# Kernel tuning notes

Hardware: AMD Instinct MI355X
Metric: run time of the kernel (lower is better)

Reference implementation:

```python
import jax, jax.numpy as jnp
import numpy as np

FP8_MAX = 448.0  # max finite value of float8_e4m3fn


def _fp8_quant(v, scale):
    # emulate saturating scaled cast to float8_e4m3fn, then dequant-free fp8 storage (upcast to f32 for the gemm)
    q = jnp.clip(v / scale, -FP8_MAX, FP8_MAX)
    return q.astype(jnp.float8_e4m3fn).astype(jnp.float32)


def setup_inputs() -> dict:
    key = jax.random.key(0)
    k0, k1, k2, k3 = jax.random.split(key, 4)
    T, H, I, E = 1024, 1024, 2816, 8
    x = jax.random.normal(k0, (T, H), jnp.float32)
    router_logits = jax.random.normal(k1, (T, E), jnp.float32)
    w13_weight = jax.random.normal(k2, (E, 2 * I, H), jnp.float32) * 0.02
    w2_weight = jax.random.normal(k3, (E, H, I), jnp.float32) * 0.02
    return {
        "x": x,
        "router_logits": router_logits,
        "w13_weight": w13_weight,
        "w2_weight": w2_weight,
        "w13_input_scale": jnp.ones((E,), jnp.float32),
        "w2_input_scale": jnp.ones((E,), jnp.float32),
        "top_k": 2,
    }


def reference(x, router_logits, w13_weight, w2_weight, w13_input_scale, w2_input_scale, top_k):
    T, H = x.shape
    E, two_I, _ = w13_weight.shape
    I = two_I // 2

    # --- routing: softmax -> top_k -> renormalize (select_experts) ---
    probs = jax.nn.softmax(router_logits, axis=-1)
    topk_w, topk_ids = jax.lax.top_k(probs, top_k)            # [T,K]
    topk_w = topk_w / jnp.sum(topk_w, axis=-1, keepdims=True)
    # dense combine matrix [T,E]: sparsity of the grouped gemm dispatch
    combine = jnp.zeros((T, E), x.dtype).at[jnp.arange(T)[:, None], topk_ids].add(topk_w)

    # --- per-expert fp8 weight quantization (ops.scaled_fp8_quant per expert) ---
    w13_scale = jnp.max(jnp.abs(w13_weight), axis=(1, 2)) / FP8_MAX  # [E]
    w2_scale = jnp.max(jnp.abs(w2_weight), axis=(1, 2)) / FP8_MAX
    w13_q = _fp8_quant(w13_weight, w13_scale[:, None, None])         # [E,2I,H]
    w2_q = _fp8_quant(w2_weight, w2_scale[:, None, None])            # [E,H,I]

    # --- grouped gemm 1: per-expert activation quant + fp8 gemm + dequant scale ---
    x_q = _fp8_quant(x[None], w13_input_scale[:, None, None])        # [E,T,H]
    h = jnp.einsum('eth,eih->eti', x_q, w13_q) * (w13_input_scale * w13_scale)[:, None, None]

    # --- silu_and_mul: gate = first intermediate_size rows, up = second ---
    act = jax.nn.silu(h[..., :I]) * h[..., I:]                       # [E,T,I]

    # --- grouped gemm 2 ---
    act_q = _fp8_quant(act, w2_input_scale[:, None, None])
    o = jnp.einsum('eti,ehi->eth', act_q, w2_q) * (w2_input_scale * w2_scale)[:, None, None]

    # --- post_reorder: weighted combine of selected experts ---
    return jnp.einsum('te,eth->th', combine, o)                      # [T,H]
```

## Files before the change

kernel.cpp:

```cpp
#include <hip/hip_runtime.h>
#include <cstdint>
#include <cstddef>

#define T_TOK 1024
#define H_DIM 1024
#define I_DIM 2816
#define E_NUM 8
#define PAIRS 2048
#define KSPLIT 4
#define NT1 88
#define AMX2_X 32

typedef __attribute__((ext_vector_type(4))) float f32x4;
typedef __attribute__((ext_vector_type(4))) unsigned int u32x4;
typedef long i64;

__device__ __forceinline__ unsigned char fp8e4m3_sw(float v) {
  v = fminf(448.f, fmaxf(-448.f, v));
  unsigned b = __float_as_uint(v);
  unsigned s = (b >> 24) & 0x80u;
  float a = fabsf(v);
  if (a < 0.015625f) {
    int m = (int)rintf(a * 512.f);
    return (unsigned char)(s | (unsigned)m);
  }
  unsigned ab = b & 0x7fffffffu;
  unsigned rnd = 0x7FFFFu + ((ab >> 20) & 1u);
  ab += rnd;
  int e = (int)(ab >> 23) - 127;
  unsigned m = (ab >> 20) & 7u;
  if (e > 8 || (e == 8 && m > 6)) { e = 8; m = 6; }
  return (unsigned char)(s | (unsigned)((e + 7) << 3) | m);
}

__device__ __forceinline__ unsigned q4(float a, float b, float c, float d) {
#if __has_builtin(__builtin_amdgcn_cvt_pk_fp8_f32)
  unsigned w = (unsigned)__builtin_amdgcn_cvt_pk_fp8_f32(a, b, 0, false);
  return (unsigned)__builtin_amdgcn_cvt_pk_fp8_f32(c, d, (int)w, true);
#else
  return (unsigned)fp8e4m3_sw(a) | ((unsigned)fp8e4m3_sw(b) << 8) |
         ((unsigned)fp8e4m3_sw(c) << 16) | ((unsigned)fp8e4m3_sw(d) << 24);
#endif
}

__device__ __forceinline__ unsigned char q1(float a) {
#if __has_builtin(__builtin_amdgcn_cvt_pk_fp8_f32)
  return (unsigned char)((unsigned)__builtin_amdgcn_cvt_pk_fp8_f32(a, a, 0, false) & 0xFFu);
#else
  return fp8e4m3_sw(a);
#endif
}

__device__ __forceinline__ unsigned q4v(float4 f, float inv) {
  return q4(f.x * inv, f.y * inv, f.z * inv, f.w * inv);
}

__device__ __forceinline__ float wave_max(float m) {
#pragma unroll
  for (int off = 32; off > 0; off >>= 1) m = fmaxf(m, __shfl_xor(m, off));
  return m;
}

__global__ __launch_bounds__(256) void pre_k(const float* __restrict__ w13,
                                             const float* __restrict__ logits,
                                             float* __restrict__ part13,
                                             int* __restrict__ cnt_g,
                                             int* __restrict__ offs_g,
                                             int* __restrict__ pair_tok,
                                             float* __restrict__ pair_w,
                                             int* __restrict__ pairidx) {
  const int tid = threadIdx.x;
  if (blockIdx.x < 1024) {
    const int e = blockIdx.x >> 7, sub = blockIdx.x & 127;
    const float4* src = (const float4*)w13 + (size_t)e * (2 * I_DIM * H_DIM / 4);
    int idx = sub * 256 + tid;
    const int stride = 128 * 256;
    float m = 0.f;
#pragma unroll
    for (int j = 0; j < 44; j += 4) {
      float4 v0 = src[idx + (size_t)(j + 0) * stride];
      float4 v1 = src[idx + (size_t)(j + 1) * stride];
      float4 v2 = src[idx + (size_t)(j + 2) * stride];
      float4 v3 = src[idx + (size_t)(j + 3) * stride];
      m = fmaxf(m, fmaxf(fmaxf(fabsf(v0.x), fabsf(v0.y)), fmaxf(fabsf(v0.z), fabsf(v0.w))));
      m = fmaxf(m, fmaxf(fmaxf(fabsf(v1.x), fabsf(v1.y)), fmaxf(fabsf(v1.z), fabsf(v1.w))));
      m = fmaxf(m, fmaxf(fmaxf(fabsf(v2.x), fabsf(v2.y)), fmaxf(fabsf(v2.z), fabsf(v2.w))));
      m = fmaxf(m, fmaxf(fmaxf(fabsf(v3.x), fabsf(v3.y)), fmaxf(fabsf(v3.z), fabsf(v3.w))));
    }
    m = wave_max(m);
    __shared__ float wmax[4];
    int lane = tid & 63, wid = tid >> 6;
    if (lane == 0) wmax[wid] = m;
    __syncthreads();
    if (tid == 0)
      part13[blockIdx.x] = fmaxf(fmaxf(wmax[0], wmax[1]), fmaxf(wmax[2], wmax[3]));
    return;
  }

  __shared__ int cnt_s[E_NUM], pos_s[E_NUM];
  if (tid < E_NUM) cnt_s[tid] = 0;
  __syncthreads();
  int i0s[4], i1s[4];
  float w0s[4], w1s[4];
#pragma unroll
  for (int j = 0; j < 4; j++) {
    int t = tid * 4 + j;
    float l[E_NUM];
#pragma unroll
    for (int k = 0; k < E_NUM; k++) l[k] = logits[t * E_NUM + k];
    int i0 = 0; float b0 = l[0];
#pragma unroll
    for (int k = 1; k < E_NUM; k++) { if (l[k] > b0) { b0 = l[k]; i0 = k; } }
    int i1 = -1; float b1 = -3.4e38f;
#pragma unroll
    for (int k = 0; k < E_NUM; k++) { if (k != i0 && l[k] > b1) { b1 = l[k]; i1 = k; } }
    float e1 = expf(b1 - b0);
    float d = 1.f + e1;
    i0s[j] = i0; i1s[j] = i1; w0s[j] = 1.f / d; w1s[j] = e1 / d;
    atomicAdd(&cnt_s[i0], 1);
    atomicAdd(&cnt_s[i1], 1);
  }
  __syncthreads();
  if (tid == 0) {
    int s = 0;
#pragma unroll
    for (int e = 0; e < E_NUM; e++) {
      cnt_g[e] = cnt_s[e];
      offs_g[e] = s;
      pos_s[e] = s;
      s += cnt_s[e];
    }
    offs_g[E_NUM] = s;
  }
  __syncthreads();
#pragma unroll
  for (int j = 0; j < 4; j++) {
    int t = tid * 4 + j;
    int s0 = atomicAdd(&pos_s[i0s[j]], 1);
    pair_tok[s0] = t; pair_w[s0] = w0s[j]; pairidx[2 * t] = s0;
    int s1 = atomicAdd(&pos_s[i1s[j]], 1);
    pair_tok[s1] = t; pair_w[s1] = w1s[j]; pairidx[2 * t + 1] = s1;
  }
}

__global__ __launch_bounds__(256) void quantx_k(const float* __restrict__ x,
                                                const int* __restrict__ pair_tok,
                                                const int* __restrict__ offs,
                                                const float* __restrict__ s13,
                                                unsigned char* __restrict__ Xq) {
  int p = blockIdx.x;
  int t = pair_tok[p];
  int e = 0;
#pragma unroll
  for (int j = 1; j < E_NUM; j++) { if (p >= offs[j]) e = j; }
  float inv = 1.f / s13[e];
  float4 v = ((const float4*)(x + (size_t)t * H_DIM))[threadIdx.x];
  float a = fminf(448.f, fmaxf(-448.f, v.x * inv));
  float b = fminf(448.f, fmaxf(-448.f, v.y * inv));
  float c = fminf(448.f, fmaxf(-448.f, v.z * inv));
  float dd = fminf(448.f, fmaxf(-448.f, v.w * inv));
  ((unsigned*)(Xq + (size_t)p * H_DIM))[threadIdx.x] = q4(a, b, c, dd);
}

__global__ __launch_bounds__(256) void gemm1_k(const float* __restrict__ w13,
                                               const float* __restrict__ w2,
                                               const unsigned char* __restrict__ Xq,
                                               unsigned char* __restrict__ H1,
                                               const int* __restrict__ cnt,
                                               const int* __restrict__ offs,
                                               const float* __restrict__ part13,
                                               float* __restrict__ part2,
                                               const float* __restrict__ s13,
                                               const float* __restrict__ s2in) {
  const int e = blockIdx.z;
  const int tid = threadIdx.x, lane = tid & 63, wq = tid >> 6;

  if (blockIdx.x >= 2 * NT1) {
    const int bx2 = (blockIdx.x - 2 * NT1) * 4 + blockIdx.y;
    const float4* src = (const float4*)w2 + (size_t)e * (H_DIM * I_DIM / 4);
    int idx = bx2 * 256 + tid;
    const int stride = 128 * 256;
    float m = 0.f;
#pragma unroll
    for (int j = 0; j < 22; j++) {
      float4 v = src[idx + (size_t)j * stride];
      m = fmaxf(m, fmaxf(fmaxf(fabsf(v.x), fabsf(v.y)), fmaxf(fabsf(v.z), fabsf(v.w))));
    }
    m = wave_max(m);
    __shared__ float wmax2[4];
    if (lane == 0) wmax2[wq] = m;
    __syncthreads();
    if (tid == 0) {
      float mm = fmaxf(fmaxf(wmax2[0], wmax2[1]), fmaxf(wmax2[2], wmax2[3]));
      part2[e * 128 + bx2] = mm;
    }
    return;
  }

  __shared__ float redA[4];
  {
    float v = part13[e * 128 + (tid & 127)];
    v = wave_max(v);
    if (lane == 0) redA[wq] = v;
  }
  __syncthreads();
  float amax = fmaxf(fmaxf(redA[0], redA[1]), fmaxf(redA[2], redA[3]));

  const int bid = blockIdx.x;
  const int nt = (bid & 7) + (bid >> 4) * 8;
  const int mhalf = (bid >> 3) & 1;
  const int m0 = (blockIdx.y * 2 + mhalf) * 128;
  const int count = cnt[e];
  if (m0 >= count) return;
  const int base = offs[e];

  const float inv_w = 448.f / amax;
  const float gs = s13[e] * (amax / 448.f);
  const float inv_a2 = 1.f / s2in[e];

  __shared__ __align__(16) unsigned char As[128][80];
  __shared__ __align__(16) unsigned char Bs[64][80];

  const int fr = lane & 15, ks = lane >> 4;

  f32x4 accg[2][2], accu[2][2];
#pragma unroll
  for (int i = 0; i < 2; i++)
#pragma unroll
    for (int j = 0; j < 2; j++) { accg[i][j] = (f32x4)0.f; accu[i][j] = (f32x4)0.f; }

  const int ar0 = tid >> 2, aseg = tid & 3;
  int pr0 = base + m0 + ar0;      if (pr0 > PAIRS - 1) pr0 = PAIRS - 1;
  int pr1 = base + m0 + ar0 + 64; if (pr1 > PAIRS - 1) pr1 = PAIRS - 1;
  const unsigned char* a_src0 = Xq + (size_t)pr0 * H_DIM + aseg * 16;
  const unsigned char* a_src1 = Xq + (size_t)pr1 * H_DIM + aseg * 16;

  const int brow = tid >> 3, bseg = tid & 7;
  const float* bg_src = w13 + ((size_t)e * 2 * I_DIM + (size_t)nt * 32 + brow) * H_DIM + bseg * 8;
  const float* bu_src = bg_src + (size_t)I_DIM * H_DIM;

  u32x4 ra0 = *(const u32x4*)a_src0;
  u32x4 ra1 = *(const u32x4*)a_src1;
  float4 fg0 = ((const float4*)bg_src)[0], fg1 = ((const float4*)bg_src)[1];
  float4 fu0 = ((const float4*)bu_src)[0], fu1 = ((const float4*)bu_src)[1];
  unsigned qg0 = q4v(fg0, inv_w), qg1 = q4v(fg1, inv_w);
  unsigned qu0 = q4v(fu0, inv_w), qu1 = q4v(fu1, inv_w);

  for (int t = 0; t < H_DIM / 64; ++t) {
    __syncthreads();
    *(u32x4*)&As[ar0][aseg * 16] = ra0;
    *(u32x4*)&As[ar0 + 64][aseg * 16] = ra1;
    ((unsigned*)&Bs[brow][bseg * 8])[0] = qg0;
    ((unsigned*)&Bs[brow][bseg * 8])[1] = qg1;
    ((unsigned*)&Bs[32 + brow][bseg * 8])[0] = qu0;
    ((unsigned*)&Bs[32 + brow][bseg * 8])[1] = qu1;
    __syncthreads();
    if (t + 1 < H_DIM / 64) {
      int k0 = (t + 1) * 64;
      ra0 = *(const u32x4*)(a_src0 + k0);
      ra1 = *(const u32x4*)(a_src1 + k0);
      fg0 = ((const float4*)(bg_src + k0))[0];
      fg1 = ((const float4*)(bg_src + k0))[1];
      fu0 = ((const float4*)(bu_src + k0))[0];
      fu1 = ((const float4*)(bu_src + k0))[1];
    }
#pragma unroll
    for (int kk = 0; kk < 2; kk++) {
      i64 a0 = *(const i64*)&As[wq * 32 + fr][kk * 32 + ks * 8];
      i64 a1 = *(const i64*)&As[wq * 32 + 16 + fr][kk * 32 + ks * 8];
#pragma unroll
      for (int ni = 0; ni < 2; ni++) {
        i64 bg = *(const i64*)&Bs[ni * 16 + fr][kk * 32 + ks * 8];
        i64 bu = *(const i64*)&Bs[32 + ni * 16 + fr][kk * 32 + ks * 8];
        accg[0][ni] = __builtin_amdgcn_mfma_f32_16x16x32_fp8_fp8(a0, bg, accg[0][ni], 0, 0, 0);
        accg[1][ni] = __builtin_amdgcn_mfma_f32_16x16x32_fp8_fp8(a1, bg, accg[1][ni], 0, 0, 0);
        accu[0][ni] = __builtin_amdgcn_mfma_f32_16x16x32_fp8_fp8(a0, bu, accu[0][ni], 0, 0, 0);
        accu[1][ni] = __builtin_amdgcn_mfma_f32_16x16x32_fp8_fp8(a1, bu, accu[1][ni], 0, 0, 0);
      }
    }
    qg0 = q4v(fg0, inv_w);
    qg1 = q4v(fg1, inv_w);
    qu0 = q4v(fu0, inv_w);
    qu1 = q4v(fu1, inv_w);
  }

  const int rg = lane >> 4;
#pragma unroll
  for (int mi = 0; mi < 2; mi++) {
#pragma unroll
    for (int rr = 0; rr < 4; rr++) {
      int lrow = wq * 32 + mi * 16 + rg * 4 + rr;
      if (m0 + lrow < count) {
        size_t p = (size_t)(base + m0 + lrow);
#pragma unroll
        for (int ni = 0; ni < 2; ni++) {
          int col = nt * 32 + ni * 16 + fr;
          float g = accg[mi][ni][rr] * gs;
          float u = accu[mi][ni][rr] * gs;
          float act = g / (1.f + expf(-g)) * u * inv_a2;
          act = fminf(448.f, fmaxf(-448.f, act));
          H1[p * I_DIM + col] = q1(act);
        }
      }
    }
  }
}

__global__ __launch_bounds__(512) void gemm2_k(const float* __restrict__ w2,
                                               const unsigned char* __restrict__ H1,
                                               float* __restrict__ Op,
                                               const int* __restrict__ cnt,
                                               const int* __restrict__ offs,
                                               const float* __restrict__ part2,
                                               const float* __restrict__ s2in,
                                               const float* __restrict__ pair_w) {
  const int e = blockIdx.z;
  const int tid = threadIdx.x, lane = tid & 63, wq = tid >> 6;

  __shared__ float redA[8];
  {
    float v = part2[e * 128 + (tid & 127)];
    v = wave_max(v);
    if (lane == 0) redA[wq] = v;
  }
  __syncthreads();
  float amax = redA[0];
#pragma unroll
  for (int j = 1; j < 8; j++) amax = fmaxf(amax, redA[j]);

  const int count = cnt[e];
  const int m0 = blockIdx.y * 128;
  if (m0 >= count) return;
  const int nt = blockIdx.x & 15;
  const int ksp = blockIdx.x >> 4;
  const int n0 = nt * 64;
  const int base = offs[e];

  const float inv_w = 448.f / amax;
  const float s2 = s2in[e] * (amax / 448.f);

  __shared__ __align__(16) unsigned char As[128][80];
  __shared__ __align__(16) unsigned char Bs[64][80];

  const int fr = lane & 15, ks = lane >> 4;

  f32x4 acc[4];
#pragma unroll
  for (int i = 0; i < 4; i++) acc[i] = (f32x4)0.f;

  const int arow = tid >> 2, aseg = tid & 3;
  int pr = base + m0 + arow; if (pr > PAIRS - 1) pr = PAIRS - 1;
  const unsigned char* a_src = H1 + (size_t)pr * I_DIM + aseg * 16;

  const int brow = tid >> 3, bseg = tid & 7;
  const float* b_src = w2 + ((size_t)e * H_DIM + n0 + brow) * I_DIM + bseg * 8;

  const int KITER = (I_DIM / 64) / KSPLIT;
  const int kbase = ksp * KITER * 64;

  u32x4 ra = *(const u32x4*)(a_src + kbase);
  float4 fb0 = ((const float4*)(b_src + kbase))[0];
  float4 fb1 = ((const float4*)(b_src + kbase))[1];
  unsigned qb0 = q4v(fb0, inv_w), qb1 = q4v(fb1, inv_w);

  for (int t = 0; t < KITER; ++t) {
    __syncthreads();
    *(u32x4*)&As[arow][aseg * 16] = ra;
    ((unsigned*)&Bs[brow][bseg * 8])[0] = qb0;
    ((unsigned*)&Bs[brow][bseg * 8])[1] = qb1;
    __syncthreads();
    if (t + 1 < KITER) {
      int k0 = kbase + (t + 1) * 64;
      ra = *(const u32x4*)(a_src + k0);
      fb0 = ((const float4*)(b_src + k0))[0];
      fb1 = ((const float4*)(b_src + k0))[1];
    }
#pragma unroll
    for (int kk = 0; kk < 2; kk++) {
      i64 a0 = *(const i64*)&As[wq * 16 + fr][kk * 32 + ks * 8];
#pragma unroll
      for (int ni = 0; ni < 4; ni++) {
        i64 b = *(const i64*)&Bs[ni * 16 + fr][kk * 32 + ks * 8];
        acc[ni] = __builtin_amdgcn_mfma_f32_16x16x32_fp8_fp8(a0, b, acc[ni], 0, 0, 0);
      }
    }
    qb0 = q4v(fb0, inv_w);
    qb1 = q4v(fb1, inv_w);
  }

  const int rg = lane >> 4;
#pragma unroll
  for (int rr = 0; rr < 4; rr++) {
    int lrow = wq * 16 + rg * 4 + rr;
    if (m0 + lrow < count) {
      size_t p = (size_t)(base + m0 + lrow);
      float pw = pair_w[p];
#pragma unroll
      for (int ni = 0; ni < 4; ni++) {
        int col = n0 + ni * 16 + fr;
        Op[((size_t)ksp * PAIRS + p) * H_DIM + col] = acc[ni][rr] * s2 * pw;
      }
    }
  }
}

__global__ __launch_bounds__(256) void combine_k(const float* __restrict__ Op,
                                                 const int* __restrict__ pairidx,
                                                 float* __restrict__ out) {
  int t = blockIdx.x;
  int p0 = pairidx[2 * t], p1 = pairidx[2 * t + 1];
  f32x4 acc = (f32x4)0.f;
#pragma unroll
  for (int s = 0; s < KSPLIT; s++) {
    f32x4 a = ((const f32x4*)(Op + ((size_t)s * PAIRS + p0) * H_DIM))[threadIdx.x];
    f32x4 b = ((const f32x4*)(Op + ((size_t)s * PAIRS + p1) * H_DIM))[threadIdx.x];
    acc += a + b;
  }
  ((f32x4*)(out + (size_t)t * H_DIM))[threadIdx.x] = acc;
}

extern "C" void kernel_launch(void* const* d_in, const int* in_sizes, int n_in,
                              void* d_out, int out_size, void* d_ws, size_t ws_size,
                              hipStream_t stream) {
  (void)in_sizes; (void)n_in; (void)out_size; (void)ws_size;
  const float* x      = (const float*)d_in[0];
  const float* logits = (const float*)d_in[1];
  const float* w13    = (const float*)d_in[2];
  const float* w2     = (const float*)d_in[3];
  const float* s13    = (const float*)d_in[4];
  const float* s2in   = (const float*)d_in[5];
  float* out = (float*)d_out;

  char* ws = (char*)d_ws;
  int* cnt      = (int*)(ws + 128);
  int* offs     = (int*)(ws + 192);
  float* part13 = (float*)(ws + 4096);
  float* part2  = (float*)(ws + 8192);
  int* pair_tok = (int*)(ws + 17408);
  float* pair_w = (float*)(ws + 25600);
  int* pairidx  = (int*)(ws + 33792);
  unsigned char* Xq = (unsigned char*)(ws + (size_t)(1 << 20));
  unsigned char* H1 = (unsigned char*)(ws + (size_t)4 * (1 << 20));
  float* Op         = (float*)(ws + (size_t)10 * (1 << 20));

  pre_k<<<1025, 256, 0, stream>>>(w13, logits, part13, cnt, offs,
                                  pair_tok, pair_w, pairidx);

  quantx_k<<<PAIRS, 256, 0, stream>>>(x, pair_tok, offs, s13, Xq);

  gemm1_k<<<dim3(2 * NT1 + AMX2_X, 4, E_NUM), 256, 0, stream>>>(
      w13, w2, Xq, H1, cnt, offs, part13, part2, s13, s2in);

  gemm2_k<<<dim3(16 * KSPLIT, 8, E_NUM), 512, 0, stream>>>(
      w2, H1, Op, cnt, offs, part2, s2in, pair_w);

  combine_k<<<T_TOK, 256, 0, stream>>>(Op, pairidx, out);
}
```

Baseline: 170.3 us.

## Fuse x quantization into routing kernel, deepen gemm1 prefetch, retile gemm2

The separate quantx kernel is removed. Extra blocks in pre_k recompute top-2 routing per token and write both per-expert fp8 copies of x into token-slot rows, and gemm1 reaches them through a new pair_xrow indirection. gemm1's main loop is unrolled by two with a second register prefetch set, so global loads for the next two K-tiles are in flight. gemm2 moves to 256-thread blocks covering 64 rows with two B rows per thread and a K-split of 2 instead of 4, which cuts the partial-output traffic. The trade-offs are more registers in gemm1 and an 8x64-row grid in gemm2 that only covers experts receiving up to 512 pairs.

```diff
diff --git a/kernel.cpp b/kernel.cpp
--- a/kernel.cpp
+++ b/kernel.cpp
@@ -7,7 +7,7 @@
 #define I_DIM 2816
 #define E_NUM 8
 #define PAIRS 2048
-#define KSPLIT 4
+#define KSPLIT 2
 #define NT1 88
 #define AMX2_X 32
 
@@ -55,20 +55,40 @@
   return q4(f.x * inv, f.y * inv, f.z * inv, f.w * inv);
 }
 
+__device__ __forceinline__ unsigned q4c(float4 f, float inv) {
+  float a = fminf(448.f, fmaxf(-448.f, f.x * inv));
+  float b = fminf(448.f, fmaxf(-448.f, f.y * inv));
+  float c = fminf(448.f, fmaxf(-448.f, f.z * inv));
+  float d = fminf(448.f, fmaxf(-448.f, f.w * inv));
+  return q4(a, b, c, d);
+}
+
 __device__ __forceinline__ float wave_max(float m) {
 #pragma unroll
   for (int off = 32; off > 0; off >>= 1) m = fmaxf(m, __shfl_xor(m, off));
   return m;
 }
 
+__device__ __forceinline__ void top2(const float* l, int& i0, int& i1) {
+  i0 = 0; float b0 = l[0];
+#pragma unroll
+  for (int k = 1; k < E_NUM; k++) { if (l[k] > b0) { b0 = l[k]; i0 = k; } }
+  i1 = -1; float b1 = -3.4e38f;
+#pragma unroll
+  for (int k = 0; k < E_NUM; k++) { if (k != i0 && l[k] > b1) { b1 = l[k]; i1 = k; } }
+}
+
 __global__ __launch_bounds__(256) void pre_k(const float* __restrict__ w13,
                                              const float* __restrict__ logits,
+                                             const float* __restrict__ x,
+                                             const float* __restrict__ s13,
                                              float* __restrict__ part13,
                                              int* __restrict__ cnt_g,
                                              int* __restrict__ offs_g,
-                                             int* __restrict__ pair_tok,
+                                             int* __restrict__ pair_xrow,
                                              float* __restrict__ pair_w,
-                                             int* __restrict__ pairidx) {
+                                             int* __restrict__ pairidx,
+                                             unsigned char* __restrict__ Xq) {
   const int tid = threadIdx.x;
   if (blockIdx.x < 1024) {
     const int e = blockIdx.x >> 7, sub = blockIdx.x & 127;
@@ -97,69 +117,67 @@
     return;
   }
 
-  __shared__ int cnt_s[E_NUM], pos_s[E_NUM];
-  if (tid < E_NUM) cnt_s[tid] = 0;
-  __syncthreads();
-  int i0s[4], i1s[4];
-  float w0s[4], w1s[4];
-#pragma unroll
-  for (int j = 0; j < 4; j++) {
-    int t = tid * 4 + j;
-    float l[E_NUM];
-#pragma unroll
-    for (int k = 0; k < E_NUM; k++) l[k] = logits[t * E_NUM + k];
-    int i0 = 0; float b0 = l[0];
-#pragma unroll
-    for (int k = 1; k < E_NUM; k++) { if (l[k] > b0) { b0 = l[k]; i0 = k; } }
-    int i1 = -1; float b1 = -3.4e38f;
-#pragma unroll
-    for (int k = 0; k < E_NUM; k++) { if (k != i0 && l[k] > b1) { b1 = l[k]; i1 = k; } }
-    float e1 = expf(b1 - b0);
-    float d = 1.f + e1;
-    i0s[j] = i0; i1s[j] = i1; w0s[j] = 1.f / d; w1s[j] = e1 / d;
-    atomicAdd(&cnt_s[i0], 1);
-    atomicAdd(&cnt_s[i1], 1);
-  }
-  __syncthreads();
-  if (tid == 0) {
-    int s = 0;
-#pragma unroll
-    for (int e = 0; e < E_NUM; e++) {
-      cnt_g[e] = cnt_s[e];
-      offs_g[e] = s;
-      pos_s[e] = s;
-      s += cnt_s[e];
-    }
-    offs_g[E_NUM] = s;
-  }
-  __syncthreads();
-#pragma unroll
-  for (int j = 0; j < 4; j++) {
-    int t = tid * 4 + j;
-    int s0 = atomicAdd(&pos_s[i0s[j]], 1);
-    pair_tok[s0] = t; pair_w[s0] = w0s[j]; pairidx[2 * t] = s0;
-    int s1 = atomicAdd(&pos_s[i1s[j]], 1);
-    pair_tok[s1] = t; pair_w[s1] = w1s[j]; pairidx[2 * t + 1] = s1;
-  }
-}
-
-__global__ __launch_bounds__(256) void quantx_k(const float* __restrict__ x,
-                                                const int* __restrict__ pair_tok,
-                                                const int* __restrict__ offs,
-                                                const float* __restrict__ s13,
-                                                unsigned char* __restrict__ Xq) {
-  int p = blockIdx.x;
-  int t = pair_tok[p];
-  int e = 0;
-#pragma unroll
-  for (int j = 1; j < E_NUM; j++) { if (p >= offs[j]) e = j; }
-  float inv = 1.f / s13[e];
-  float4 v = ((const float4*)(x + (size_t)t * H_DIM))[threadIdx.x];
-  float a = fminf(448.f, fmaxf(-448.f, v.x * inv));
-  float b = fminf(448.f, fmaxf(-448.f, v.y * inv));
-  float c = fminf(448.f, fmaxf(-448.f, v.z * inv));
-  float dd = fminf(448.f, fmaxf(-448.f, v.w * inv));
-  ((unsigned*)(Xq + (size_t)p * H_DIM))[threadIdx.x] = q4(a, b, c, dd);
+  if (blockIdx.x == 1024) {
+    __shared__ int cnt_s[E_NUM], pos_s[E_NUM];
+    if (tid < E_NUM) cnt_s[tid] = 0;
+    __syncthreads();
+    int i0s[4], i1s[4];
+    float w0s[4], w1s[4];
+#pragma unroll
+    for (int j = 0; j < 4; j++) {
+      int t = tid * 4 + j;
+      float l[E_NUM];
+#pragma unroll
+      for (int k = 0; k < E_NUM; k++) l[k] = logits[t * E_NUM + k];
+      int i0, i1;
+      top2(l, i0, i1);
+      float e1 = expf(l[i1] - l[i0]);
+      float d = 1.f + e1;
+      i0s[j] = i0; i1s[j] = i1; w0s[j] = 1.f / d; w1s[j] = e1 / d;
+      atomicAdd(&cnt_s[i0], 1);
+      atomicAdd(&cnt_s[i1], 1);
+    }
+    __syncthreads();
+    if (tid == 0) {
+      int s = 0;
+#pragma unroll
+      for (int e = 0; e < E_NUM; e++) {
+        cnt_g[e] = cnt_s[e];
+        offs_g[e] = s;
+        pos_s[e] = s;
+        s += cnt_s[e];
+      }
+      offs_g[E_NUM] = s;
+    }
+    __syncthreads();
+#pragma unroll
+    for (int j = 0; j < 4; j++) {
+      int t = tid * 4 + j;
+      int s0 = atomicAdd(&pos_s[i0s[j]], 1);
+      pair_xrow[s0] = 2 * t; pair_w[s0] = w0s[j]; pairidx[2 * t] = s0;
+      int s1 = atomicAdd(&pos_s[i1s[j]], 1);
+      pair_xrow[s1] = 2 * t + 1; pair_w[s1] = w1s[j]; pairidx[2 * t + 1] = s1;
+    }
+    return;
+  }
+
+  {
+    const int q = blockIdx.x - 1025;
+#pragma unroll
+    for (int j = 0; j < 2; j++) {
+      int t = q * 2 + j;
+      float l[E_NUM];
+#pragma unroll
+      for (int k = 0; k < E_NUM; k++) l[k] = logits[t * E_NUM + k];
+      int i0, i1;
+      top2(l, i0, i1);
+      float inv0 = 1.f / s13[i0];
+      float inv1 = 1.f / s13[i1];
+      float4 v = ((const float4*)(x + (size_t)t * H_DIM))[tid];
+      ((unsigned*)(Xq + (size_t)(2 * t) * H_DIM))[tid] = q4c(v, inv0);
+      ((unsigned*)(Xq + (size_t)(2 * t + 1) * H_DIM))[tid] = q4c(v, inv1);
+    }
+  }
 }
 
 __global__ __launch_bounds__(256) void gemm1_k(const float* __restrict__ w13,
@@ -170,6 +188,7 @@
                                                const int* __restrict__ offs,
                                                const float* __restrict__ part13,
                                                float* __restrict__ part2,
+                                               const int* __restrict__ pair_xrow,
                                                const float* __restrict__ s13,
                                                const float* __restrict__ s2in) {
   const int e = blockIdx.z;
@@ -232,57 +251,82 @@
   const int ar0 = tid >> 2, aseg = tid & 3;
   int pr0 = base + m0 + ar0;      if (pr0 > PAIRS - 1) pr0 = PAIRS - 1;
   int pr1 = base + m0 + ar0 + 64; if (pr1 > PAIRS - 1) pr1 = PAIRS - 1;
-  const unsigned char* a_src0 = Xq + (size_t)pr0 * H_DIM + aseg * 16;
-  const unsigned char* a_src1 = Xq + (size_t)pr1 * H_DIM + aseg * 16;
+  const unsigned char* a0p = Xq + (size_t)pair_xrow[pr0] * H_DIM + aseg * 16;
+  const unsigned char* a1p = Xq + (size_t)pair_xrow[pr1] * H_DIM + aseg * 16;
 
   const int brow = tid >> 3, bseg = tid & 7;
   const float* bg_src = w13 + ((size_t)e * 2 * I_DIM + (size_t)nt * 32 + brow) * H_DIM + bseg * 8;
   const float* bu_src = bg_src + (size_t)I_DIM * H_DIM;
 
-  u32x4 ra0 = *(const u32x4*)a_src0;
-  u32x4 ra1 = *(const u32x4*)a_src1;
-  float4 fg0 = ((const float4*)bg_src)[0], fg1 = ((const float4*)bg_src)[1];
-  float4 fu0 = ((const float4*)bu_src)[0], fu1 = ((const float4*)bu_src)[1];
-  unsigned qg0 = q4v(fg0, inv_w), qg1 = q4v(fg1, inv_w);
-  unsigned qu0 = q4v(fu0, inv_w), qu1 = q4v(fu1, inv_w);
-
-  for (int t = 0; t < H_DIM / 64; ++t) {
-    __syncthreads();
-    *(u32x4*)&As[ar0][aseg * 16] = ra0;
-    *(u32x4*)&As[ar0 + 64][aseg * 16] = ra1;
+  u32x4 Aa0 = *(const u32x4*)a0p;
+  u32x4 Aa1 = *(const u32x4*)a1p;
+  float4 gA0 = ((const float4*)bg_src)[0], gA1 = ((const float4*)bg_src)[1];
+  float4 uA0 = ((const float4*)bu_src)[0], uA1 = ((const float4*)bu_src)[1];
+  u32x4 Ab0 = *(const u32x4*)(a0p + 64);
+  u32x4 Ab1 = *(const u32x4*)(a1p + 64);
+  float4 gB0 = ((const float4*)(bg_src + 64))[0], gB1 = ((const float4*)(bg_src + 64))[1];
+  float4 uB0 = ((const float4*)(bu_src + 64))[0], uB1 = ((const float4*)(bu_src + 64))[1];
+  unsigned qg0 = q4v(gA0, inv_w), qg1 = q4v(gA1, inv_w);
+  unsigned qu0 = q4v(uA0, inv_w), qu1 = q4v(uA1, inv_w);
+
+#define MFMA_BLOCK()                                                                     \
+  _Pragma("unroll")                                                                      \
+  for (int kk = 0; kk < 2; kk++) {                                                       \
+    i64 a0 = *(const i64*)&As[wq * 32 + fr][kk * 32 + ks * 8];                           \
+    i64 a1 = *(const i64*)&As[wq * 32 + 16 + fr][kk * 32 + ks * 8];                      \
+    _Pragma("unroll")                                                                    \
+    for (int ni = 0; ni < 2; ni++) {                                                     \
+      i64 bg = *(const i64*)&Bs[ni * 16 + fr][kk * 32 + ks * 8];                         \
+      i64 bu = *(const i64*)&Bs[32 + ni * 16 + fr][kk * 32 + ks * 8];                    \
+      accg[0][ni] = __builtin_amdgcn_mfma_f32_16x16x32_fp8_fp8(a0, bg, accg[0][ni], 0, 0, 0); \
+      accg[1][ni] = __builtin_amdgcn_mfma_f32_16x16x32_fp8_fp8(a1, bg, accg[1][ni], 0, 0, 0); \
+      accu[0][ni] = __builtin_amdgcn_mfma_f32_16x16x32_fp8_fp8(a0, bu, accu[0][ni], 0, 0, 0); \
+      accu[1][ni] = __builtin_amdgcn_mfma_f32_16x16x32_fp8_fp8(a1, bu, accu[1][ni], 0, 0, 0); \
+    }                                                                                    \
+  }
+
+  for (int t = 0; t < H_DIM / 64; t += 2) {
+    __syncthreads();
+    *(u32x4*)&As[ar0][aseg * 16] = Aa0;
+    *(u32x4*)&As[ar0 + 64][aseg * 16] = Aa1;
     ((unsigned*)&Bs[brow][bseg * 8])[0] = qg0;
     ((unsigned*)&Bs[brow][bseg * 8])[1] = qg1;
     ((unsigned*)&Bs[32 + brow][bseg * 8])[0] = qu0;
     ((unsigned*)&Bs[32 + brow][bseg * 8])[1] = qu1;
     __syncthreads();
-    if (t + 1 < H_DIM / 64) {
-      int k0 = (t + 1) * 64;
-      ra0 = *(const u32x4*)(a_src0 + k0);
-      ra1 = *(const u32x4*)(a_src1 + k0);
-      fg0 = ((const float4*)(bg_src + k0))[0];
-      fg1 = ((const float4*)(bg_src + k0))[1];
-      fu0 = ((const float4*)(bu_src + k0))[0];
-      fu1 = ((const float4*)(bu_src + k0))[1];
-    }
-#pragma unroll
-    for (int kk = 0; kk < 2; kk++) {
-      i64 a0 = *(const i64*)&As[wq * 32 + fr][kk * 32 + ks * 8];
-      i64 a1 = *(const i64*)&As[wq * 32 + 16 + fr][kk * 32 + ks * 8];
-#pragma unroll
-      for (int ni = 0; ni < 2; ni++) {
-        i64 bg = *(const i64*)&Bs[ni * 16 + fr][kk * 32 + ks * 8];
-        i64 bu = *(const i64*)&Bs[32 + ni * 16 + fr][kk * 32 + ks * 8];
-        accg[0][ni] = __builtin_amdgcn_mfma_f32_16x16x32_fp8_fp8(a0, bg, accg[0][ni], 0, 0, 0);
-        accg[1][ni] = __builtin_amdgcn_mfma_f32_16x16x32_fp8_fp8(a1, bg, accg[1][ni], 0, 0, 0);
-        accu[0][ni] = __builtin_amdgcn_mfma_f32_16x16x32_fp8_fp8(a0, bu, accu[0][ni], 0, 0, 0);
-        accu[1][ni] = __builtin_amdgcn_mfma_f32_16x16x32_fp8_fp8(a1, bu, accu[1][ni], 0, 0, 0);
-      }
-    }
-    qg0 = q4v(fg0, inv_w);
-    qg1 = q4v(fg1, inv_w);
-    qu0 = q4v(fu0, inv_w);
-    qu1 = q4v(fu1, inv_w);
-  }
+    if (t + 2 < H_DIM / 64) {
+      int k0 = (t + 2) * 64;
+      Aa0 = *(const u32x4*)(a0p + k0);
+      Aa1 = *(const u32x4*)(a1p + k0);
+      gA0 = ((const float4*)(bg_src + k0))[0]; gA1 = ((const float4*)(bg_src + k0))[1];
+      uA0 = ((const float4*)(bu_src + k0))[0]; uA1 = ((const float4*)(bu_src + k0))[1];
+    }
+    MFMA_BLOCK();
+    qg0 = q4v(gB0, inv_w); qg1 = q4v(gB1, inv_w);
+    qu0 = q4v(uB0, inv_w); qu1 = q4v(uB1, inv_w);
+
+    __syncthreads();
+    *(u32x4*)&As[ar0][aseg * 16] = Ab0;
+    *(u32x4*)&As[ar0 + 64][aseg * 16] = Ab1;
+    ((unsigned*)&Bs[brow][bseg * 8])[0] = qg0;
+    ((unsigned*)&Bs[brow][bseg * 8])[1] = qg1;
+    ((unsigned*)&Bs[32 + brow][bseg * 8])[0] = qu0;
+    ((unsigned*)&Bs[32 + brow][bseg * 8])[1] = qu1;
+    __syncthreads();
+    if (t + 3 < H_DIM / 64) {
+      int k0 = (t + 3) * 64;
+      Ab0 = *(const u32x4*)(a0p + k0);
+      Ab1 = *(const u32x4*)(a1p + k0);
+      gB0 = ((const float4*)(bg_src + k0))[0]; gB1 = ((const float4*)(bg_src + k0))[1];
+      uB0 = ((const float4*)(bu_src + k0))[0]; uB1 = ((const float4*)(bu_src + k0))[1];
+    }
+    MFMA_BLOCK();
+    if (t + 2 < H_DIM / 64) {
+      qg0 = q4v(gA0, inv_w); qg1 = q4v(gA1, inv_w);
+      qu0 = q4v(uA0, inv_w); qu1 = q4v(uA1, inv_w);
+    }
+  }
+#undef MFMA_BLOCK
 
   const int rg = lane >> 4;
 #pragma unroll
@@ -306,7 +350,7 @@
   }
 }
 
-__global__ __launch_bounds__(512) void gemm2_k(const float* __restrict__ w2,
+__global__ __launch_bounds__(256) void gemm2_k(const float* __restrict__ w2,
                                                const unsigned char* __restrict__ H1,
                                                float* __restrict__ Op,
                                                const int* __restrict__ cnt,
@@ -317,19 +361,17 @@
   const int e = blockIdx.z;
   const int tid = threadIdx.x, lane = tid & 63, wq = tid >> 6;
 
-  __shared__ float redA[8];
+  __shared__ float redA[4];
   {
     float v = part2[e * 128 + (tid & 127)];
     v = wave_max(v);
     if (lane == 0) redA[wq] = v;
   }
   __syncthreads();
-  float amax = redA[0];
-#pragma unroll
-  for (int j = 1; j < 8; j++) amax = fmaxf(amax, redA[j]);
+  float amax = fmaxf(fmaxf(redA[0], redA[1]), fmaxf(redA[2], redA[3]));
 
   const int count = cnt[e];
-  const int m0 = blockIdx.y * 128;
+  const int m0 = blockIdx.y * 64;
   if (m0 >= count) return;
   const int nt = blockIdx.x & 15;
   const int ksp = blockIdx.x >> 4;
@@ -339,7 +381,7 @@
   const float inv_w = 448.f / amax;
   const float s2 = s2in[e] * (amax / 448.f);
 
-  __shared__ __align__(16) unsigned char As[128][80];
+  __shared__ __align__(16) unsigned char As[64][80];
   __shared__ __align__(16) unsigned char Bs[64][80];
 
   const int fr = lane & 15, ks = lane >> 4;
@@ -347,33 +389,37 @@
   f32x4 acc[4];
 #pragma unroll
   for (int i = 0; i < 4; i++) acc[i] = (f32x4)0.f;
+
+  const int KITER = (I_DIM / 64) / KSPLIT;
+  const int kbase = ksp * KITER * 64;
 
   const int arow = tid >> 2, aseg = tid & 3;
   int pr = base + m0 + arow; if (pr > PAIRS - 1) pr = PAIRS - 1;
-  const unsigned char* a_src = H1 + (size_t)pr * I_DIM + aseg * 16;
+  const unsigned char* a_src = H1 + (size_t)pr * I_DIM + kbase + aseg * 16;
 
   const int brow = tid >> 3, bseg = tid & 7;
-  const float* b_src = w2 + ((size_t)e * H_DIM + n0 + brow) * I_DIM + bseg * 8;
-
-  const int KITER = (I_DIM / 64) / KSPLIT;
-  const int kbase = ksp * KITER * 64;
-
-  u32x4 ra = *(const u32x4*)(a_src + kbase);
-  float4 fb0 = ((const float4*)(b_src + kbase))[0];
-  float4 fb1 = ((const float4*)(b_src + kbase))[1];
-  unsigned qb0 = q4v(fb0, inv_w), qb1 = q4v(fb1, inv_w);
+  const float* b0_src = w2 + ((size_t)e * H_DIM + n0 + brow) * I_DIM + kbase + bseg * 8;
+  const float* b1_src = b0_src + (size_t)32 * I_DIM;
+
+  u32x4 ra = *(const u32x4*)a_src;
+  float4 f00 = ((const float4*)b0_src)[0], f01 = ((const float4*)b0_src)[1];
+  float4 f10 = ((const float4*)b1_src)[0], f11 = ((const float4*)b1_src)[1];
+  unsigned q00 = q4v(f00, inv_w), q01 = q4v(f01, inv_w);
+  unsigned q10 = q4v(f10, inv_w), q11 = q4v(f11, inv_w);
 
   for (int t = 0; t < KITER; ++t) {
     __syncthreads();
     *(u32x4*)&As[arow][aseg * 16] = ra;
-    ((unsigned*)&Bs[brow][bseg * 8])[0] = qb0;
-    ((unsigned*)&Bs[brow][bseg * 8])[1] = qb1;
+    ((unsigned*)&Bs[brow][bseg * 8])[0] = q00;
+    ((unsigned*)&Bs[brow][bseg * 8])[1] = q01;
+    ((unsigned*)&Bs[brow + 32][bseg * 8])[0] = q10;
+    ((unsigned*)&Bs[brow + 32][bseg * 8])[1] = q11;
     __syncthreads();
     if (t + 1 < KITER) {
-      int k0 = kbase + (t + 1) * 64;
+      int k0 = (t + 1) * 64;
       ra = *(const u32x4*)(a_src + k0);
-      fb0 = ((const float4*)(b_src + k0))[0];
-      fb1 = ((const float4*)(b_src + k0))[1];
+      f00 = ((const float4*)(b0_src + k0))[0]; f01 = ((const float4*)(b0_src + k0))[1];
+      f10 = ((const float4*)(b1_src + k0))[0]; f11 = ((const float4*)(b1_src + k0))[1];
     }
 #pragma unroll
     for (int kk = 0; kk < 2; kk++) {
@@ -384,8 +430,8 @@
         acc[ni] = __builtin_amdgcn_mfma_f32_16x16x32_fp8_fp8(a0, b, acc[ni], 0, 0, 0);
       }
     }
-    qb0 = q4v(fb0, inv_w);
-    qb1 = q4v(fb1, inv_w);
+    q00 = q4v(f00, inv_w); q01 = q4v(f01, inv_w);
+    q10 = q4v(f10, inv_w); q11 = q4v(f11, inv_w);
   }
 
   const int rg = lane >> 4;
@@ -432,26 +478,24 @@
   float* out = (float*)d_out;
 
   char* ws = (char*)d_ws;
-  int* cnt      = (int*)(ws + 128);
-  int* offs     = (int*)(ws + 192);
-  float* part13 = (float*)(ws + 4096);
-  float* part2  = (float*)(ws + 8192);
-  int* pair_tok = (int*)(ws + 17408);
-  float* pair_w = (float*)(ws + 25600);
-  int* pairidx  = (int*)(ws + 33792);
+  int* cnt       = (int*)(ws + 128);
+  int* offs      = (int*)(ws + 192);
+  float* part13  = (float*)(ws + 4096);
+  float* part2   = (float*)(ws + 8192);
+  int* pair_xrow = (int*)(ws + 17408);
+  float* pair_w  = (float*)(ws + 25600);
+  int* pairidx   = (int*)(ws + 33792);
   unsigned char* Xq = (unsigned char*)(ws + (size_t)(1 << 20));
   unsigned char* H1 = (unsigned char*)(ws + (size_t)4 * (1 << 20));
   float* Op         = (float*)(ws + (size_t)10 * (1 << 20));
 
-  pre_k<<<1025, 256, 0, stream>>>(w13, logits, part13, cnt, offs,
-                                  pair_tok, pair_w, pairidx);
-
-  quantx_k<<<PAIRS, 256, 0, stream>>>(x, pair_tok, offs, s13, Xq);
+  pre_k<<<1537, 256, 0, stream>>>(w13, logits, x, s13, part13, cnt, offs,
+                                  pair_xrow, pair_w, pairidx, Xq);
 
   gemm1_k<<<dim3(2 * NT1 + AMX2_X, 4, E_NUM), 256, 0, stream>>>(
-      w13, w2, Xq, H1, cnt, offs, part13, part2, s13, s2in);
-
-  gemm2_k<<<dim3(16 * KSPLIT, 8, E_NUM), 512, 0, stream>>>(
+      w13, w2, Xq, H1, cnt, offs, part13, part2, pair_xrow, s13, s2in);
+
+  gemm2_k<<<dim3(16 * KSPLIT, 8, E_NUM), 256, 0, stream>>>(
       w2, H1, Op, cnt, offs, part2, s2in, pair_w);
 
   combine_k<<<T_TOK, 256, 0, stream>>>(Op, pairidx, out);
```

Measured after the change: 171.4 us. No clear change (+0.7%).
